# Performance work log

Measured on AMD Instinct MI355X. Metric: run time of the kernel, lower is better.

The kernel has to match this reference:

```python
import jax, jax.numpy as jnp
import numpy as np

B, I, O, DEG = 16384, 1024, 1024, 8

def setup_inputs() -> dict:
    key = jax.random.key(0)
    kx, kc = jax.random.split(key)
    x = jax.random.normal(kx, (B, I), dtype=jnp.float32)
    std = 1.0 / (I * (DEG + 1))
    cheby_coeffs = jax.random.normal(kc, (I, O, DEG + 1), dtype=jnp.float32) * std
    return {"x": x, "cheby_coeffs": cheby_coeffs}


def reference(x, cheby_coeffs):
    # Chebyshev basis: T_d(tanh(x)) = cos(d * acos(tanh(x)))
    deg = cheby_coeffs.shape[-1]
    arange = jnp.arange(deg, dtype=x.dtype)  # (D+1,)
    theta = jnp.arccos(jnp.tanh(x))          # (B, I)
    basis = jnp.cos(theta[:, :, None] * arange)  # (B, I, D+1)
    y = jnp.einsum('bid,iod->bo', basis, cheby_coeffs)
    return y
```

## Files before the change

### kernel.cpp

```cpp
#include <hip/hip_runtime.h>
#include <hip/hip_bf16.h>


#define WSCALE 4096.0f
#define INV_WSCALE (1.0f/4096.0f)

typedef _Float16 f16;
typedef __fp16   hf2  __attribute__((ext_vector_type(2)));
typedef _Float16 f16x2v __attribute__((ext_vector_type(2)));
typedef _Float16 f16x8 __attribute__((ext_vector_type(8)));
typedef float    f32x4 __attribute__((ext_vector_type(4)));
typedef float    f32x4u __attribute__((ext_vector_type(4), aligned(4)));
typedef float    f32x2u __attribute__((ext_vector_type(2), aligned(4)));
typedef float    f32x16 __attribute__((ext_vector_type(16)));

union F16x8u { hf2 h2[4]; f16x8 v8; };

__global__ __launch_bounds__(256) void wt_transform(const float* __restrict__ cc,
                                                    f16* __restrict__ wt) {
  __shared__ f16 s16[9216];
  const int bid  = blockIdx.x;
  const int u    = bid & 3;
  const int ncol = (bid >> 2) & 7;
  const int ic   = bid >> 5;
  const int t    = threadIdx.x;
  const int i2   = t >> 4;
  const int o2   = t & 15;
  const int i0   = i2 * 2, o0 = o2 * 2;
  const int h    = i0 >> 4;
  const int kl   = (i0 >> 3) & 1;
  const int e    = i0 & 7;

  float va[2][18];
#pragma unroll
  for (int ii = 0; ii < 2; ++ii) {
    const float* g = cc + ((size_t)(ic * 32 + i0 + ii) * 1024
                           + (ncol * 128 + u * 32 + o0)) * 9;
    f32x4u a = *(const f32x4u*)(g);
    f32x4u b = *(const f32x4u*)(g + 4);
    f32x4u c4 = *(const f32x4u*)(g + 8);
    f32x4u d4 = *(const f32x4u*)(g + 12);
    f32x2u e2 = *(const f32x2u*)(g + 16);
#pragma unroll
    for (int j = 0; j < 4; ++j) { va[ii][j] = a[j]; va[ii][4 + j] = b[j];
                                  va[ii][8 + j] = c4[j]; va[ii][12 + j] = d4[j]; }
    va[ii][16] = e2[0]; va[ii][17] = e2[1];
  }

#pragma unroll
  for (int oo = 0; oo < 2; ++oo) {
    const int ol = o0 + oo;
    const int r  = ol & 15, q = ol >> 4;
    const int rk = (r >> 1) & 3;
    const int vsl = (kl * 2 + q) ^ rk;
    const int jj = h * 16 + r;
#pragma unroll
    for (int d = 0; d < 9; ++d) {
      f16x2v pv = { (f16)(va[0][oo * 9 + d] * WSCALE),
                    (f16)(va[1][oo * 9 + d] * WSCALE) };
      *(f16x2v*)(&s16[(d * 128 + jj * 4 + vsl) * 8 + e]) = pv;
    }
  }
  __syncthreads();

#pragma unroll
  for (int w = 0; w < 5; ++w) {
    int cidx = t + 256 * w;
    if (cidx < 1152) {
      f16x8 val = *(const f16x8*)(&s16[cidx * 8]);
      int d = cidx >> 7, rem = cidx & 127;
      *(f16x8*)(wt + (size_t)((d * 32 + ic) * 8 + ncol) * 4096 + u * 1024 + rem * 8) = val;
    }
  }
}

__global__ __launch_bounds__(256) void t2_transform(const float* __restrict__ x,
                                                    f16* __restrict__ t2) {
  size_t gid = (size_t)blockIdx.x * 256 + threadIdx.x;
  const float* p = x + gid * 8;
  f32x4 a = *(const f32x4*)p;
  f32x4 b = *(const f32x4*)(p + 4);
  float tf[8];
#pragma unroll
  for (int e = 0; e < 8; ++e) {
    float xx = (e < 4) ? a[e] : b[e - 4];
    tf[e] = 1.f - 2.f * __builtin_amdgcn_rcpf(__expf(2.f * xx) + 1.f);
  }
  F16x8u u;
#pragma unroll
  for (int q = 0; q < 4; ++q)
    u.h2[q] = __builtin_amdgcn_cvt_pkrtz(tf[2 * q], tf[2 * q + 1]);
  f16x8 v = u.v8 + u.v8;
  *(f16x8*)(t2 + gid * 8) = v;
}

__global__ __launch_bounds__(256, 3) void cheby_gemm(const f16* __restrict__ t2g,
                                                     const f16* __restrict__ wt,
                                                     float* __restrict__ out) {
  __shared__ f16 bbuf[6][4096];

  const int tid  = threadIdx.x;
  const int wid  = tid >> 6;
  const int lane = tid & 63;
  const int lr   = lane & 31;
  const int lh   = lane >> 5;
  const int wm   = wid >> 1;
  const int wn   = wid & 1;
  const int mrow = blockIdx.x >> 3;
  const int ncol = blockIdx.x & 7;
  const int m0   = mrow * 128 + wm * 64;
  const int n0   = ncol * 128 + wn * 64;
  const int rbase = wn * 2048 + ((lane & 15) * 4 + ((lane >> 4) ^ ((lane >> 1) & 3))) * 8;

  auto stage = [&](int cn, int dn, int slot) {
    const f16* src = wt + (size_t)(dn * 32 + cn) * 32768 + (size_t)ncol * 4096;
    __builtin_amdgcn_global_load_lds(
        (const __attribute__((address_space(1))) unsigned*)(src + tid * 8),
        (__attribute__((address_space(3))) unsigned*)(&bbuf[slot][wid * 512]),
        16, 0, 0);
    __builtin_amdgcn_global_load_lds(
        (const __attribute__((address_space(1))) unsigned*)(src + 2048 + tid * 8),
        (__attribute__((address_space(3))) unsigned*)(&bbuf[slot][wid * 512 + 2048]),
        16, 0, 0);
  };

  f32x16 acc[2][2];
#pragma unroll
  for (int a = 0; a < 2; ++a)
#pragma unroll
    for (int b = 0; b < 2; ++b)
#pragma unroll
      for (int j = 0; j < 16; ++j) acc[a][b][j] = 0.f;

  const f16x8 ones  = {(f16)1,(f16)1,(f16)1,(f16)1,(f16)1,(f16)1,(f16)1,(f16)1};
  const f16x8 half8 = {(f16)0.5f,(f16)0.5f,(f16)0.5f,(f16)0.5f,
                       (f16)0.5f,(f16)0.5f,(f16)0.5f,(f16)0.5f};
  f16x8 t2v[2][2], t2n[2][2];

  auto loadx = [&](int cn) {
#pragma unroll
    for (int mb = 0; mb < 2; ++mb)
#pragma unroll
      for (int h = 0; h < 2; ++h)
        t2n[mb][h] = *(const f16x8*)(t2g + (size_t)(m0 + mb * 32 + lr) * 1024
                                         + cn * 32 + h * 16 + lh * 8);
  };

#define REC(NEW, S1, S2)                                                       \
  _Pragma("unroll") for (int mb = 0; mb < 2; ++mb)                             \
    _Pragma("unroll") for (int h = 0; h < 2; ++h)                              \
      NEW[mb][h] = __builtin_elementwise_fma(t2v[mb][h], S1[mb][h], -S2[mb][h]);

#define LB(BD, SLOT)                                                           \
  {                                                                            \
    const f16* bb = &bbuf[0][0] + (SLOT) * 4096 + rbase;                       \
    BD[0][0] = *(const f16x8*)&bb[0];    BD[0][1] = *(const f16x8*)&bb[512];   \
    BD[1][0] = *(const f16x8*)&bb[1024]; BD[1][1] = *(const f16x8*)&bb[1536];  \
  }

#define M8(AF, BD)                                                             \
  {                                                                            \
    _Pragma("unroll") for (int nb = 0; nb < 2; ++nb)                           \
      _Pragma("unroll") for (int mb = 0; mb < 2; ++mb) {                       \
        acc[mb][nb] = __builtin_amdgcn_mfma_f32_32x32x16_f16(AF[mb][0], BD[nb][0], \
                                                             acc[mb][nb], 0, 0, 0); \
        acc[mb][nb] = __builtin_amdgcn_mfma_f32_32x32x16_f16(AF[mb][1], BD[nb][1], \
                                                             acc[mb][nb], 0, 0, 0); \
      }                                                                        \
  }

#define ADOPT                                                                  \
  _Pragma("unroll") for (int mb = 0; mb < 2; ++mb)                             \
    _Pragma("unroll") for (int h = 0; h < 2; ++h) {                            \
      t2v[mb][h] = t2n[mb][h];                                                 \
      A1[mb][h]  = t2v[mb][h] * half8;                                         \
    }

#define VMB(N)                                                                 \
  asm volatile("s_waitcnt vmcnt(" #N ")" ::: "memory");                        \
  __builtin_amdgcn_s_barrier();

  f16x8 onesA[2][2];
#pragma unroll
  for (int mb = 0; mb < 2; ++mb)
#pragma unroll
    for (int h = 0; h < 2; ++h) onesA[mb][h] = ones;

  f16x8 bf0[2][2], bf1[2][2], bf2[2][2];
  f16x8 A1[2][2], A2[2][2], A3[2][2], A4[2][2], A5[2][2], A6[2][2], A7[2][2], A8[2][2];
  int q0 = 0, q1 = 1, q2 = 2, q3 = 3, q4 = 4, q5 = 5;

  loadx(0);
  stage(0, 0, 0); stage(0, 1, 1); stage(0, 2, 2); stage(0, 3, 3); stage(0, 4, 4);
  VMB(6)
  LB(bf0, 0) LB(bf1, 1)

  VMB(4)
  LB(bf2, q2)
  ADOPT
  stage(0, 5, q5);
  M8(onesA, bf0)

  for (int c = 0; c < 31; ++c) {
    VMB(4) stage(c, 6, q0); loadx(c + 1); LB(bf0, q3) REC(A2, A1, onesA) M8(A1, bf1)
    VMB(8) stage(c, 7, q1);     LB(bf1, q4) REC(A3, A2, A1) M8(A2, bf2)
    VMB(8) stage(c, 8, q2);     LB(bf2, q5) REC(A4, A3, A2) M8(A3, bf0)
    VMB(8) stage(c + 1, 0, q3); LB(bf0, q0) REC(A5, A4, A3) M8(A4, bf1)
    VMB(4) stage(c + 1, 1, q4); LB(bf1, q1) REC(A6, A5, A4) M8(A5, bf2)
    VMB(4) stage(c + 1, 2, q5); LB(bf2, q2) REC(A7, A6, A5) M8(A6, bf0)
    VMB(4) stage(c + 1, 3, q0); LB(bf0, q3) REC(A8, A7, A6) M8(A7, bf1)
    VMB(4) stage(c + 1, 4, q1); LB(bf1, q4)                 M8(A8, bf2)
    { int r0 = q0, r1 = q1, r2 = q2;
      q0 = q3; q1 = q4; q2 = q5; q3 = r0; q4 = r1; q5 = r2; }
    VMB(4)
    LB(bf2, q2)
    ADOPT
    stage(c + 1, 5, q5);
    M8(onesA, bf0)
  }

  VMB(4) stage(31, 6, q0); LB(bf0, q3) REC(A2, A1, onesA) M8(A1, bf1)
  VMB(4) stage(31, 7, q1); LB(bf1, q4) REC(A3, A2, A1)    M8(A2, bf2)
  VMB(4) stage(31, 8, q2); LB(bf2, q5) REC(A4, A3, A2)    M8(A3, bf0)
  VMB(4) LB(bf0, q0) REC(A5, A4, A3) M8(A4, bf1)
  VMB(2) LB(bf1, q1) REC(A6, A5, A4) M8(A5, bf2)
  VMB(0) LB(bf2, q2) REC(A7, A6, A5) M8(A6, bf0)
  REC(A8, A7, A6) M8(A7, bf1)
  M8(A8, bf2)

#undef REC
#undef LB
#undef M8
#undef ADOPT
#undef VMB

#pragma unroll
  for (int mb = 0; mb < 2; ++mb)
#pragma unroll
    for (int nb = 0; nb < 2; ++nb)
#pragma unroll
      for (int j = 0; j < 16; ++j) {
        int row = m0 + mb * 32 + 4 * lh + (j & 3) + 8 * (j >> 2);
        int col = n0 + nb * 32 + lr;
        out[(size_t)row * 1024 + col] = acc[mb][nb][j] * INV_WSCALE;
      }
}

__global__ __launch_bounds__(512, 2) void cheby_gemm_fb(const float* __restrict__ x,
                                                        const f16* __restrict__ wt,
                                                        float* __restrict__ out) {
  __shared__ f16 bbuf[18][4096];
  const int tid  = threadIdx.x;
  const int wid  = tid >> 6;
  const int lane = tid & 63;
  const int lr   = lane & 31;
  const int lh   = lane >> 5;
  const int wm   = wid >> 1;
  const int wn   = wid & 1;
  const int mrow = blockIdx.x >> 3;
  const int ncol = blockIdx.x & 7;
  const int m0   = mrow * 256 + wm * 64;
  const int n0   = ncol * 128 + wn * 64;
  const int rbase = wn * 2048 + ((lane & 15) * 4 + ((lane >> 4) ^ ((lane >> 1) & 3))) * 8;

  auto stage = [&](int cn, int dn, int buf) {
    const f16* src = wt + (size_t)(dn * 32 + cn) * 32768 + (size_t)ncol * 4096;
    __builtin_amdgcn_global_load_lds(
        (const __attribute__((address_space(1))) unsigned*)(src + tid * 8),
        (__attribute__((address_space(3))) unsigned*)(&bbuf[buf][wid * 512]),
        16, 0, 0);
  };
  auto stage9 = [&](int cn, int b0) {
#pragma unroll
    for (int d = 0; d < 9; ++d) stage(cn, d, b0 + d);
  };

  f32x16 acc[2][2];
#pragma unroll
  for (int a = 0; a < 2; ++a)
#pragma unroll
    for (int b = 0; b < 2; ++b)
#pragma unroll
      for (int j = 0; j < 16; ++j) acc[a][b][j] = 0.f;

  const f16x8 ones  = {(f16)1,(f16)1,(f16)1,(f16)1,(f16)1,(f16)1,(f16)1,(f16)1};
  const f16x8 half8 = {(f16)0.5f,(f16)0.5f,(f16)0.5f,(f16)0.5f,
                       (f16)0.5f,(f16)0.5f,(f16)0.5f,(f16)0.5f};
  f16x8 t2v[2][2], t2n[2][2];
  f32x4 xf[2][2][2];

  auto loadx = [&](int cn) {
#pragma unroll
    for (int mb = 0; mb < 2; ++mb)
#pragma unroll
      for (int h = 0; h < 2; ++h) {
        const float* p = x + (size_t)(m0 + mb * 32 + lr) * 1024 + cn * 32 + h * 16 + lh * 8;
        xf[mb][h][0] = *(const f32x4*)p;
        xf[mb][h][1] = *(const f32x4*)(p + 4);
      }
  };
  auto dotanh = [&]() {
#pragma unroll
    for (int mb = 0; mb < 2; ++mb)
#pragma unroll
      for (int h = 0; h < 2; ++h) {
        float tf[8];
#pragma unroll
        for (int e = 0; e < 8; ++e) {
          float xx = (e < 4) ? xf[mb][h][0][e] : xf[mb][h][1][e - 4];
          tf[e] = 1.f - 2.f * __builtin_amdgcn_rcpf(__expf(2.f * xx) + 1.f);
        }
        F16x8u u;
#pragma unroll
        for (int q = 0; q < 4; ++q)
          u.h2[q] = __builtin_amdgcn_cvt_pkrtz(tf[2 * q], tf[2 * q + 1]);
        t2n[mb][h] = u.v8 + u.v8;
      }
  };

#define REC(NEW, S1, S2)                                                       \
  _Pragma("unroll") for (int mb = 0; mb < 2; ++mb)                             \
    _Pragma("unroll") for (int h = 0; h < 2; ++h)                              \
      NEW[mb][h] = __builtin_elementwise_fma(t2v[mb][h], S1[mb][h], -S2[mb][h]);
#define CLUSTER(AF, DIDX)                                                      \
  {                                                                            \
    const f16* bb = &bbuf[0][0] + sbase + (DIDX) * 4096 + rbase;               \
    f16x8 bf[2][2];                                                            \
    _Pragma("unroll") for (int nb = 0; nb < 2; ++nb)                           \
      _Pragma("unroll") for (int h = 0; h < 2; ++h)                            \
        bf[nb][h] = *(const f16x8*)&bb[nb * 1024 + h * 512];                   \
    _Pragma("unroll") for (int nb = 0; nb < 2; ++nb)                           \
      _Pragma("unroll") for (int mb = 0; mb < 2; ++mb) {                       \
        acc[mb][nb] = __builtin_amdgcn_mfma_f32_32x32x16_f16(AF[mb][0], bf[nb][0], \
                                                             acc[mb][nb], 0, 0, 0); \
        acc[mb][nb] = __builtin_amdgcn_mfma_f32_32x32x16_f16(AF[mb][1], bf[nb][1], \
                                                             acc[mb][nb], 0, 0, 0); \
      }                                                                        \
  }

  stage9(0, 0);
  loadx(0);
  dotanh();

  f16x8 onesA[2][2];
#pragma unroll
  for (int mb = 0; mb < 2; ++mb)
#pragma unroll
    for (int h = 0; h < 2; ++h) onesA[mb][h] = ones;

  for (int c = 0; c < 32; ++c) {
    const bool lastc = (c == 31);
    const int  sbase = (c & 1) * 36864;
    const int  nbase = (1 - (c & 1)) * 9;

    asm volatile("s_waitcnt vmcnt(8)" ::: "memory");
    __builtin_amdgcn_s_barrier();

    f16x8 A1[2][2], A2[2][2], A3[2][2], A4[2][2], A5[2][2], A6[2][2], A7[2][2], A8[2][2];
#pragma unroll
    for (int mb = 0; mb < 2; ++mb)
#pragma unroll
      for (int h = 0; h < 2; ++h) {
        t2v[mb][h] = t2n[mb][h];
        A1[mb][h]  = t2v[mb][h] * half8;
      }
    if (!lastc) { stage9(c + 1, nbase); loadx(c + 1); }

    CLUSTER(onesA, 0)
    CLUSTER(A1, 1)
    REC(A2, A1, onesA)  CLUSTER(A2, 2)
    REC(A3, A2, A1)     CLUSTER(A3, 3)
    REC(A4, A3, A2)     CLUSTER(A4, 4)
    REC(A5, A4, A3)     CLUSTER(A5, 5)
    REC(A6, A5, A4)     CLUSTER(A6, 6)
    REC(A7, A6, A5)     CLUSTER(A7, 7)
    REC(A8, A7, A6)     CLUSTER(A8, 8)
    if (!lastc) dotanh();
  }
#undef REC
#undef CLUSTER

#pragma unroll
  for (int mb = 0; mb < 2; ++mb)
#pragma unroll
    for (int nb = 0; nb < 2; ++nb)
#pragma unroll
      for (int j = 0; j < 16; ++j) {
        int row = m0 + mb * 32 + 4 * lh + (j & 3) + 8 * (j >> 2);
        int col = n0 + nb * 32 + lr;
        out[(size_t)row * 1024 + col] = acc[mb][nb][j] * INV_WSCALE;
      }
}

extern "C" void kernel_launch(void* const* d_in, const int* in_sizes, int n_in,
                              void* d_out, int out_size, void* d_ws, size_t ws_size,
                              hipStream_t stream) {
  const float* x  = (const float*)d_in[0];
  const float* cc = (const float*)d_in[1];
  f16*   wt  = (f16*)d_ws;
  f16*   t2  = (f16*)((char*)d_ws + 18874368);
  float* out = (float*)d_out;

  hipLaunchKernelGGL(wt_transform, dim3(1024), dim3(256), 0, stream, cc, wt);
  if (ws_size >= 52428800) {
    hipLaunchKernelGGL(t2_transform, dim3(8192), dim3(256), 0, stream, x, t2);
    hipLaunchKernelGGL(cheby_gemm, dim3(1024), dim3(256), 0, stream, t2, wt, out);
  } else {
    hipLaunchKernelGGL(cheby_gemm_fb, dim3(512), dim3(512), 0, stream, x, wt, out);
  }
}
```

Baseline: 301.0 us.

## Shrink LDS ring to five slots and two B-fragment registers for four waves/SIMD

Reduces the shared-memory B staging ring from six to five slots and the register-held B fragments from three to two sets. It also drops the separate next-chunk x register buffer, loading x directly into the current buffer. Together these cut LDS and VGPR use so the launch bound can be raised from 3 to 4 blocks per CU, aiming for more latency hiding. In exchange the pipeline is rescheduled with a shallower prefetch distance and some extra barriers, and the x load is no longer overlapped with the previous chunk.

```diff
diff --git a/kernel.cpp b/kernel.cpp
--- a/kernel.cpp
+++ b/kernel.cpp
@@ -94,10 +94,10 @@
   *(f16x8*)(t2 + gid * 8) = v;
 }
 
-__global__ __launch_bounds__(256, 3) void cheby_gemm(const f16* __restrict__ t2g,
+__global__ __launch_bounds__(256, 4) void cheby_gemm(const f16* __restrict__ t2g,
                                                      const f16* __restrict__ wt,
                                                      float* __restrict__ out) {
-  __shared__ f16 bbuf[6][4096];
+  __shared__ f16 bbuf[5][4096];
 
   const int tid  = threadIdx.x;
   const int wid  = tid >> 6;
@@ -135,14 +135,14 @@
   const f16x8 ones  = {(f16)1,(f16)1,(f16)1,(f16)1,(f16)1,(f16)1,(f16)1,(f16)1};
   const f16x8 half8 = {(f16)0.5f,(f16)0.5f,(f16)0.5f,(f16)0.5f,
                        (f16)0.5f,(f16)0.5f,(f16)0.5f,(f16)0.5f};
-  f16x8 t2v[2][2], t2n[2][2];
+  f16x8 t2v[2][2];
 
   auto loadx = [&](int cn) {
 #pragma unroll
     for (int mb = 0; mb < 2; ++mb)
 #pragma unroll
       for (int h = 0; h < 2; ++h)
-        t2n[mb][h] = *(const f16x8*)(t2g + (size_t)(m0 + mb * 32 + lr) * 1024
+        t2v[mb][h] = *(const f16x8*)(t2g + (size_t)(m0 + mb * 32 + lr) * 1024
                                          + cn * 32 + h * 16 + lh * 8);
   };
 
@@ -171,10 +171,8 @@
 
 #define ADOPT                                                                  \
   _Pragma("unroll") for (int mb = 0; mb < 2; ++mb)                             \
-    _Pragma("unroll") for (int h = 0; h < 2; ++h) {                            \
-      t2v[mb][h] = t2n[mb][h];                                                 \
-      A1[mb][h]  = t2v[mb][h] * half8;                                         \
-    }
+    _Pragma("unroll") for (int h = 0; h < 2; ++h)                              \
+      A1[mb][h] = t2v[mb][h] * half8;
 
 #define VMB(N)                                                                 \
   asm volatile("s_waitcnt vmcnt(" #N ")" ::: "memory");                        \
@@ -186,48 +184,56 @@
 #pragma unroll
     for (int h = 0; h < 2; ++h) onesA[mb][h] = ones;
 
-  f16x8 bf0[2][2], bf1[2][2], bf2[2][2];
+  f16x8 bfA[2][2], bfB[2][2];
   f16x8 A1[2][2], A2[2][2], A3[2][2], A4[2][2], A5[2][2], A6[2][2], A7[2][2], A8[2][2];
-  int q0 = 0, q1 = 1, q2 = 2, q3 = 3, q4 = 4, q5 = 5;
-
-  loadx(0);
-  stage(0, 0, 0); stage(0, 1, 1); stage(0, 2, 2); stage(0, 3, 3); stage(0, 4, 4);
-  VMB(6)
-  LB(bf0, 0) LB(bf1, 1)
-
-  VMB(4)
-  LB(bf2, q2)
-  ADOPT
-  stage(0, 5, q5);
-  M8(onesA, bf0)
+  int p0 = 0, p1 = 1, p2 = 2, p3 = 3, p4 = 4;
+
+  stage(0, 0, p0); stage(0, 1, p1); stage(0, 2, p2); stage(0, 3, p3);
 
   for (int c = 0; c < 31; ++c) {
-    VMB(4) stage(c, 6, q0); loadx(c + 1); LB(bf0, q3) REC(A2, A1, onesA) M8(A1, bf1)
-    VMB(8) stage(c, 7, q1);     LB(bf1, q4) REC(A3, A2, A1) M8(A2, bf2)
-    VMB(8) stage(c, 8, q2);     LB(bf2, q5) REC(A4, A3, A2) M8(A3, bf0)
-    VMB(8) stage(c + 1, 0, q3); LB(bf0, q0) REC(A5, A4, A3) M8(A4, bf1)
-    VMB(4) stage(c + 1, 1, q4); LB(bf1, q1) REC(A6, A5, A4) M8(A5, bf2)
-    VMB(4) stage(c + 1, 2, q5); LB(bf2, q2) REC(A7, A6, A5) M8(A6, bf0)
-    VMB(4) stage(c + 1, 3, q0); LB(bf0, q3) REC(A8, A7, A6) M8(A7, bf1)
-    VMB(4) stage(c + 1, 4, q1); LB(bf1, q4)                 M8(A8, bf2)
-    { int r0 = q0, r1 = q1, r2 = q2;
-      q0 = q3; q1 = q4; q2 = q5; q3 = r0; q4 = r1; q5 = r2; }
     VMB(4)
-    LB(bf2, q2)
+    LB(bfA, p0)
+    loadx(c);
+    stage(c, 4, p4);
     ADOPT
-    stage(c + 1, 5, q5);
-    M8(onesA, bf0)
-  }
-
-  VMB(4) stage(31, 6, q0); LB(bf0, q3) REC(A2, A1, onesA) M8(A1, bf1)
-  VMB(4) stage(31, 7, q1); LB(bf1, q4) REC(A3, A2, A1)    M8(A2, bf2)
-  VMB(4) stage(31, 8, q2); LB(bf2, q5) REC(A4, A3, A2)    M8(A3, bf0)
-  VMB(4) LB(bf0, q0) REC(A5, A4, A3) M8(A4, bf1)
-  VMB(2) LB(bf1, q1) REC(A6, A5, A4) M8(A5, bf2)
-  VMB(0) LB(bf2, q2) REC(A7, A6, A5) M8(A6, bf0)
-  REC(A8, A7, A6) M8(A7, bf1)
-  M8(A8, bf2)
-
+    LB(bfB, p1)
+    M8(onesA, bfA)
+
+    __builtin_amdgcn_s_barrier();
+    stage(c, 5, p0); LB(bfA, p2) REC(A2, A1, onesA) M8(A1, bfB)
+    __builtin_amdgcn_s_barrier();
+    stage(c, 6, p1); LB(bfB, p3) REC(A3, A2, A1)    M8(A2, bfA)
+    VMB(4) stage(c, 7, p2); LB(bfA, p4) REC(A4, A3, A2) M8(A3, bfB)
+    VMB(4) stage(c, 8, p3); LB(bfB, p0) REC(A5, A4, A3) M8(A4, bfA)
+    VMB(4) stage(c + 1, 0, p4); LB(bfA, p1) REC(A6, A5, A4) M8(A5, bfB)
+    VMB(4) stage(c + 1, 1, p0); LB(bfB, p2) REC(A7, A6, A5) M8(A6, bfA)
+    VMB(4) stage(c + 1, 2, p1); LB(bfA, p3) REC(A8, A7, A6) M8(A7, bfB)
+    stage(c + 1, 3, p2);
+    M8(A8, bfA)
+
+    int tmp = p4; p4 = p3; p3 = p2; p2 = p1; p1 = p0; p0 = tmp;
+  }
+
+  {
+    VMB(4)
+    LB(bfA, p0)
+    loadx(31);
+    stage(31, 4, p4);
+    ADOPT
+    LB(bfB, p1)
+    M8(onesA, bfA)
+
+    __builtin_amdgcn_s_barrier();
+    stage(31, 5, p0); LB(bfA, p2) REC(A2, A1, onesA) M8(A1, bfB)
+    __builtin_amdgcn_s_barrier();
+    stage(31, 6, p1); LB(bfB, p3) REC(A3, A2, A1)    M8(A2, bfA)
+    VMB(4) stage(31, 7, p2); LB(bfA, p4) REC(A4, A3, A2) M8(A3, bfB)
+    VMB(4) stage(31, 8, p3); LB(bfB, p0) REC(A5, A4, A3) M8(A4, bfA)
+    VMB(4) LB(bfA, p1) REC(A6, A5, A4) M8(A5, bfB)
+    VMB(2) LB(bfB, p2) REC(A7, A6, A5) M8(A6, bfA)
+    VMB(0) LB(bfA, p3) REC(A8, A7, A6) M8(A7, bfB)
+    M8(A8, bfA)
+  }
 #undef REC
 #undef LB
 #undef M8
```

After: 398.8 us. 32.5% more time.

## Fold degree-zero Chebyshev term into precomputed bias, drop its GEMM chunk

Applied to the files above, without the earlier changes.

Because T_0 equals one, the degree-zero contribution is simply a per-output sum of coefficients over the inputs. A small kernel now precomputes that sum into a bias vector, and the GEMM epilogue adds it. This removes one of nine MFMA passes per input chunk and the matching weight staging, and the LDS ring shrinks from six slots to five. The cost is an extra launch with strided reads of the coefficient array, plus fp32 bias summation, which changes accumulation order compared with the fp16 MFMA path.

```diff
diff --git a/kernel.cpp b/kernel.cpp
--- a/kernel.cpp
+++ b/kernel.cpp
@@ -94,10 +94,33 @@
   *(f16x8*)(t2 + gid * 8) = v;
 }
 
+__global__ __launch_bounds__(256) void bias_kernel(const float* __restrict__ cc,
+                                                   float* __restrict__ bias) {
+  __shared__ float red[256];
+  const int t  = threadIdx.x;
+  const int ol = t >> 4;
+  const int sl = t & 15;
+  const int o  = blockIdx.x * 16 + ol;
+  float s = 0.f;
+  const float* p = cc + (size_t)(sl * 64) * 9216 + (size_t)o * 9;
+#pragma unroll 4
+  for (int i = 0; i < 64; ++i) s += p[(size_t)i * 9216];
+  red[t] = s;
+  __syncthreads();
+  if (sl < 8) red[t] += red[t + 8];
+  __syncthreads();
+  if (sl < 4) red[t] += red[t + 4];
+  __syncthreads();
+  if (sl < 2) red[t] += red[t + 2];
+  __syncthreads();
+  if (sl == 0) bias[o] = red[t] + red[t + 1];
+}
+
 __global__ __launch_bounds__(256, 3) void cheby_gemm(const f16* __restrict__ t2g,
                                                      const f16* __restrict__ wt,
+                                                     const float* __restrict__ bias,
                                                      float* __restrict__ out) {
-  __shared__ f16 bbuf[6][4096];
+  __shared__ f16 bbuf[5][4096];
 
   const int tid  = threadIdx.x;
   const int wid  = tid >> 6;
@@ -186,54 +209,60 @@
 #pragma unroll
     for (int h = 0; h < 2; ++h) onesA[mb][h] = ones;
 
-  f16x8 bf0[2][2], bf1[2][2], bf2[2][2];
+  f16x8 bfA[2][2], bfB[2][2];
   f16x8 A1[2][2], A2[2][2], A3[2][2], A4[2][2], A5[2][2], A6[2][2], A7[2][2], A8[2][2];
-  int q0 = 0, q1 = 1, q2 = 2, q3 = 3, q4 = 4, q5 = 5;
+  int s1 = 0, s2 = 1, s3 = 2, s4 = 3, s5 = 4;
 
   loadx(0);
-  stage(0, 0, 0); stage(0, 1, 1); stage(0, 2, 2); stage(0, 3, 3); stage(0, 4, 4);
-  VMB(6)
-  LB(bf0, 0) LB(bf1, 1)
-
-  VMB(4)
-  LB(bf2, q2)
-  ADOPT
-  stage(0, 5, q5);
-  M8(onesA, bf0)
+  stage(0, 1, s1); stage(0, 2, s2); stage(0, 3, s3); stage(0, 4, s4);
 
   for (int c = 0; c < 31; ++c) {
-    VMB(4) stage(c, 6, q0); loadx(c + 1); LB(bf0, q3) REC(A2, A1, onesA) M8(A1, bf1)
-    VMB(8) stage(c, 7, q1);     LB(bf1, q4) REC(A3, A2, A1) M8(A2, bf2)
-    VMB(8) stage(c, 8, q2);     LB(bf2, q5) REC(A4, A3, A2) M8(A3, bf0)
-    VMB(8) stage(c + 1, 0, q3); LB(bf0, q0) REC(A5, A4, A3) M8(A4, bf1)
-    VMB(4) stage(c + 1, 1, q4); LB(bf1, q1) REC(A6, A5, A4) M8(A5, bf2)
-    VMB(4) stage(c + 1, 2, q5); LB(bf2, q2) REC(A7, A6, A5) M8(A6, bf0)
-    VMB(4) stage(c + 1, 3, q0); LB(bf0, q3) REC(A8, A7, A6) M8(A7, bf1)
-    VMB(4) stage(c + 1, 4, q1); LB(bf1, q4)                 M8(A8, bf2)
-    { int r0 = q0, r1 = q1, r2 = q2;
-      q0 = q3; q1 = q4; q2 = q5; q3 = r0; q4 = r1; q5 = r2; }
     VMB(4)
-    LB(bf2, q2)
+    LB(bfA, s1)
     ADOPT
-    stage(c + 1, 5, q5);
-    M8(onesA, bf0)
-  }
-
-  VMB(4) stage(31, 6, q0); LB(bf0, q3) REC(A2, A1, onesA) M8(A1, bf1)
-  VMB(4) stage(31, 7, q1); LB(bf1, q4) REC(A3, A2, A1)    M8(A2, bf2)
-  VMB(4) stage(31, 8, q2); LB(bf2, q5) REC(A4, A3, A2)    M8(A3, bf0)
-  VMB(4) LB(bf0, q0) REC(A5, A4, A3) M8(A4, bf1)
-  VMB(2) LB(bf1, q1) REC(A6, A5, A4) M8(A5, bf2)
-  VMB(0) LB(bf2, q2) REC(A7, A6, A5) M8(A6, bf0)
-  REC(A8, A7, A6) M8(A7, bf1)
-  M8(A8, bf2)
-
+    stage(c, 5, s5);
+    loadx(c + 1);
+    LB(bfB, s2)
+    M8(A1, bfA)
+
+    VMB(8) stage(c, 6, s1); LB(bfA, s3) REC(A2, A1, onesA) M8(A2, bfB)
+    VMB(8) stage(c, 7, s2); LB(bfB, s4) REC(A3, A2, A1)    M8(A3, bfA)
+    VMB(8) stage(c, 8, s3); LB(bfA, s5) REC(A4, A3, A2)    M8(A4, bfB)
+    VMB(4) stage(c + 1, 1, s4); LB(bfB, s1) REC(A5, A4, A3) M8(A5, bfA)
+    VMB(4) stage(c + 1, 2, s5); LB(bfA, s2) REC(A6, A5, A4) M8(A6, bfB)
+    VMB(4) stage(c + 1, 3, s1); LB(bfB, s3) REC(A7, A6, A5) M8(A7, bfA)
+    stage(c + 1, 4, s2);
+    REC(A8, A7, A6) M8(A8, bfB)
+
+    { int n1 = s4, n2 = s5, n3 = s1, n4 = s2, n5 = s3;
+      s1 = n1; s2 = n2; s3 = n3; s4 = n4; s5 = n5; }
+  }
+
+  {
+    VMB(4)
+    LB(bfA, s1)
+    ADOPT
+    stage(31, 5, s5);
+    LB(bfB, s2)
+    M8(A1, bfA)
+
+    VMB(4) stage(31, 6, s1); LB(bfA, s3) REC(A2, A1, onesA) M8(A2, bfB)
+    VMB(4) stage(31, 7, s2); LB(bfB, s4) REC(A3, A2, A1)    M8(A3, bfA)
+    VMB(4) stage(31, 8, s3); LB(bfA, s5) REC(A4, A3, A2)    M8(A4, bfB)
+    VMB(4) LB(bfB, s1) REC(A5, A4, A3) M8(A5, bfA)
+    VMB(2) LB(bfA, s2) REC(A6, A5, A4) M8(A6, bfB)
+    VMB(0) LB(bfB, s3) REC(A7, A6, A5) M8(A7, bfA)
+    REC(A8, A7, A6) M8(A8, bfB)
+  }
 #undef REC
 #undef LB
 #undef M8
 #undef ADOPT
 #undef VMB
 
+  float bno[2];
+  bno[0] = bias[n0 + lr];
+  bno[1] = bias[n0 + 32 + lr];
 #pragma unroll
   for (int mb = 0; mb < 2; ++mb)
 #pragma unroll
@@ -242,7 +271,7 @@
       for (int j = 0; j < 16; ++j) {
         int row = m0 + mb * 32 + 4 * lh + (j & 3) + 8 * (j >> 2);
         int col = n0 + nb * 32 + lr;
-        out[(size_t)row * 1024 + col] = acc[mb][nb][j] * INV_WSCALE;
+        out[(size_t)row * 1024 + col] = acc[mb][nb][j] * INV_WSCALE + bno[nb];
       }
 }
 
@@ -397,14 +426,16 @@
                               hipStream_t stream) {
   const float* x  = (const float*)d_in[0];
   const float* cc = (const float*)d_in[1];
-  f16*   wt  = (f16*)d_ws;
-  f16*   t2  = (f16*)((char*)d_ws + 18874368);
-  float* out = (float*)d_out;
+  f16*   wt   = (f16*)d_ws;
+  f16*   t2   = (f16*)((char*)d_ws + 18874368);
+  float* bias = (float*)((char*)d_ws + 52428800);
+  float* out  = (float*)d_out;
 
   hipLaunchKernelGGL(wt_transform, dim3(1024), dim3(256), 0, stream, cc, wt);
-  if (ws_size >= 52428800) {
+  if (ws_size >= 52432896) {
     hipLaunchKernelGGL(t2_transform, dim3(8192), dim3(256), 0, stream, x, t2);
-    hipLaunchKernelGGL(cheby_gemm, dim3(1024), dim3(256), 0, stream, t2, wt, out);
+    hipLaunchKernelGGL(bias_kernel, dim3(64), dim3(256), 0, stream, cc, bias);
+    hipLaunchKernelGGL(cheby_gemm, dim3(1024), dim3(256), 0, stream, t2, wt, bias, out);
   } else {
     hipLaunchKernelGGL(cheby_gemm_fb, dim3(512), dim3(512), 0, stream, x, wt, out);
   }
```

New measurement: 292.5 us. -2.8%, faster.
